# Kernel optimization log

Hardware: AMD Instinct MI355X
Metric: run time of the kernel (lower is better)

Reference implementation:

```python
import jax, jax.numpy as jnp
import numpy as np

K_TOP = 200          # hard-coded topk k in source
FEAT_OUT = 16080     # hard-coded scatter / output feature width in source


def setup_inputs() -> dict:
    key = jax.random.key(0)
    k1, k2 = jax.random.split(key)
    x = jax.random.normal(k1, (256, 120, 134), dtype=jnp.float32)
    # Parameter initialized uniform_(-1, 1) in the original module
    attention_mask = jax.random.uniform(k2, (64, 1000), dtype=jnp.float32, minval=-1.0, maxval=1.0)
    return {"x": x, "attention_mask": attention_mask}


def reference(x, attention_mask):
    B = x.shape[0]
    T = attention_mask.shape[0]  # number_of_trees
    x2 = x.reshape(B, -1)  # (B, 16080)
    att_tmp = jax.nn.sigmoid(attention_mask)               # (T, 1000)
    topk, idx = jax.lax.top_k(att_tmp, K_TOP)              # (T, 200) each
    # scatter_(-1, idx, topk) into zeros(T, 16080); idx values < 1000
    attention = jnp.zeros((T, FEAT_OUT), dtype=x.dtype)
    attention = attention.at[jnp.arange(T)[:, None], idx].set(topk)  # (T, 16080)
    # per-tree broadcast multiply, fused into one batched outer broadcast
    return_value = x2[:, None, :] * attention[None, :, :]  # (B, T, 16080)
    return (return_value, attention)
```

## Files before the change

kernel.cpp:

```cpp
#include <hip/hip_runtime.h>

typedef float v4f __attribute__((ext_vector_type(4)));

constexpr int B = 256;
constexpr int T = 64;
constexpr int C = 1000;
constexpr int F = 16080;
constexpr int K = 200;
constexpr int F4 = F / 4;
constexpr int C4 = C / 4;
constexpr unsigned N4 = (unsigned)B * T * F4;

__global__ __launch_bounds__(256) void topk_scatter_kernel(
    const float* __restrict__ mask, float* __restrict__ attn) {
  const int t = blockIdx.x;
  const int tid = threadIdx.x;
  __shared__ unsigned long long keys[1024];

  const float* row = mask + (size_t)t * C;
  float* arow = attn + (size_t)t * F;

  for (int i = tid; i < 1024; i += 256) {
    if (i < C) {
      unsigned ub = __float_as_uint(row[i]);
      unsigned mono = (ub & 0x80000000u) ? ~ub : (ub | 0x80000000u);
      keys[i] = ((unsigned long long)mono << 32) | (unsigned)(~i);
    } else {
      keys[i] = 0ull;
    }
  }
  {
    v4f* arow4 = (v4f*)arow;
    const v4f z = {0.0f, 0.0f, 0.0f, 0.0f};
    for (int i = tid; i < F4; i += 256) arow4[i] = z;
  }
  __syncthreads();

  for (int k = 2; k <= 1024; k <<= 1) {
    for (int j = k >> 1; j > 0; j >>= 1) {
      for (int ii = tid; ii < 1024; ii += 256) {
        int l = ii ^ j;
        if (l > ii) {
          unsigned long long a = keys[ii];
          unsigned long long b2 = keys[l];
          bool sw = ((ii & k) == 0) ? (a < b2) : (a > b2);
          if (sw) { keys[ii] = b2; keys[l] = a; }
        }
      }
      __syncthreads();
    }
  }

  if (tid < K) {
    unsigned long long key = keys[tid];
    unsigned idx = ~(unsigned)(key & 0xFFFFFFFFull);
    unsigned mono = (unsigned)(key >> 32);
    unsigned bits = (mono & 0x80000000u) ? (mono ^ 0x80000000u) : ~mono;
    float v = __uint_as_float(bits);
    float s = 1.0f / (1.0f + expf(-v));
    arow[idx] = s;
  }
}

__global__ __launch_bounds__(256) void flat_outer_kernel(
    const float* __restrict__ x, const float* __restrict__ attn,
    float* __restrict__ out) {
  const v4f* __restrict__ x4 = (const v4f*)x;
  const v4f* __restrict__ a4 = (const v4f*)attn;
  v4f* __restrict__ o4 = (v4f*)out;

  const unsigned stride = gridDim.x * 256u;
  for (unsigned i = blockIdx.x * 256u + threadIdx.x; i < N4; i += stride) {
    unsigned p = i / (unsigned)F4;
    unsigned c = i - p * (unsigned)F4;
    v4f v = {0.0f, 0.0f, 0.0f, 0.0f};
    if (c < (unsigned)C4) {
      unsigned b = p >> 6;
      unsigned t = p & 63u;
      v = x4[b * (unsigned)F4 + c] * a4[t * (unsigned)F4 + c];
    }
    o4[i] = v;
  }
}

extern "C" void kernel_launch(void* const* d_in, const int* in_sizes, int n_in,
                              void* d_out, int out_size, void* d_ws, size_t ws_size,
                              hipStream_t stream) {
  const float* x = (const float*)d_in[0];
  const float* mask = (const float*)d_in[1];
  float* out = (float*)d_out;
  float* attn = out + (size_t)B * T * F;

  topk_scatter_kernel<<<T, 256, 0, stream>>>(mask, attn);
  flat_outer_kernel<<<8192, 256, 0, stream>>>(x, attn, out);
}
```

Before: 1.093 ms.

## Zero output with memset and compute only the nonzero attention columns

After: 1.066 ms. 1.03x faster.

```diff
diff --git a/kernel.cpp b/kernel.cpp
--- a/kernel.cpp
+++ b/kernel.cpp
@@ -9,7 +9,7 @@
 constexpr int K = 200;
 constexpr int F4 = F / 4;
 constexpr int C4 = C / 4;
-constexpr unsigned N4 = (unsigned)B * T * F4;
+constexpr unsigned ND = (unsigned)B * T * C4;
 
 __global__ __launch_bounds__(256) void topk_scatter_kernel(
     const float* __restrict__ mask, float* __restrict__ attn) {
@@ -18,7 +18,6 @@
   __shared__ unsigned long long keys[1024];
 
   const float* row = mask + (size_t)t * C;
-  float* arow = attn + (size_t)t * F;
 
   for (int i = tid; i < 1024; i += 256) {
     if (i < C) {
@@ -28,11 +27,6 @@
     } else {
       keys[i] = 0ull;
     }
-  }
-  {
-    v4f* arow4 = (v4f*)arow;
-    const v4f z = {0.0f, 0.0f, 0.0f, 0.0f};
-    for (int i = tid; i < F4; i += 256) arow4[i] = z;
   }
   __syncthreads();
 
@@ -58,11 +52,11 @@
     unsigned bits = (mono & 0x80000000u) ? (mono ^ 0x80000000u) : ~mono;
     float v = __uint_as_float(bits);
     float s = 1.0f / (1.0f + expf(-v));
-    arow[idx] = s;
+    attn[(size_t)t * F + idx] = s;
   }
 }
 
-__global__ __launch_bounds__(256) void flat_outer_kernel(
+__global__ __launch_bounds__(256) void dense_kernel(
     const float* __restrict__ x, const float* __restrict__ attn,
     float* __restrict__ out) {
   const v4f* __restrict__ x4 = (const v4f*)x;
@@ -70,16 +64,12 @@
   v4f* __restrict__ o4 = (v4f*)out;
 
   const unsigned stride = gridDim.x * 256u;
-  for (unsigned i = blockIdx.x * 256u + threadIdx.x; i < N4; i += stride) {
-    unsigned p = i / (unsigned)F4;
-    unsigned c = i - p * (unsigned)F4;
-    v4f v = {0.0f, 0.0f, 0.0f, 0.0f};
-    if (c < (unsigned)C4) {
-      unsigned b = p >> 6;
-      unsigned t = p & 63u;
-      v = x4[b * (unsigned)F4 + c] * a4[t * (unsigned)F4 + c];
-    }
-    o4[i] = v;
+  for (unsigned j = blockIdx.x * 256u + threadIdx.x; j < ND; j += stride) {
+    unsigned row = j / (unsigned)C4;
+    unsigned c = j - row * (unsigned)C4;
+    unsigned b = row >> 6;
+    unsigned t = row & 63u;
+    o4[(size_t)row * F4 + c] = x4[b * (unsigned)F4 + c] * a4[t * (unsigned)F4 + c];
   }
 }
 
@@ -91,6 +81,10 @@
   float* out = (float*)d_out;
   float* attn = out + (size_t)B * T * F;
 
+  const size_t total_bytes = ((size_t)B * T + (size_t)T) * (size_t)F * sizeof(float);
+  hipMemsetAsync(d_out, 0, total_bytes, stream);
+
   topk_scatter_kernel<<<T, 256, 0, stream>>>(mask, attn);
-  flat_outer_kernel<<<8192, 256, 0, stream>>>(x, attn, out);
+
+  dense_kernel<<<2048, 256, 0, stream>>>(x, attn, out);
 }
```
